# Kernel optimization log

Hardware: AMD Instinct MI355X
Metric: run time of the kernel (lower is better)

## Reference

```python
import jax, jax.numpy as jnp
import numpy as np

NUM_HEADS = 16
LN_EPS = 1e-5
ROPE_BASE = 10000.0


def setup_inputs() -> dict:
    key = jax.random.key(0)
    ks = jax.random.split(key, 4)
    B, T, D = 2, 2048, 1024
    return {
        "x": jax.random.normal(ks[0], (B, T, D), jnp.float32),
        "in_proj_weight": jax.random.normal(ks[1], (3 * D, D), jnp.float32) * 0.02,
        "in_proj_bias": jnp.zeros((3 * D,), jnp.float32),
        "out_proj_weight": jax.random.normal(ks[2], (D, D), jnp.float32) * 0.02,
        "out_proj_bias": jnp.zeros((D,), jnp.float32),
        "ln_gamma": jnp.ones((D,), jnp.float32),
        "ln_beta": jnp.zeros((D,), jnp.float32),
    }


def _rope_cos_sin(T, head_dim):
    # standard rotary tables; apply_rotary in the source truncates the
    # concatenated (T, head_dim) tables back to (T, head_dim//2), so we
    # build the half-width tables directly.
    inv_freq = 1.0 / (ROPE_BASE ** (jnp.arange(0, head_dim, 2, dtype=jnp.float32) / head_dim))
    t = jnp.arange(T, dtype=jnp.float32)
    freqs = jnp.outer(t, inv_freq)  # (T, head_dim//2)
    return jnp.cos(freqs), jnp.sin(freqs)


def _apply_rotary(x, cos, sin):
    # x: (B, H, T, hD), split-half rotary variant
    x1, x2 = jnp.split(x, 2, axis=-1)
    cos = cos[None, None]
    sin = sin[None, None]
    return jnp.concatenate([x1 * cos - x2 * sin, x2 * cos + x1 * sin], axis=-1).astype(x.dtype)


def reference(x, in_proj_weight, in_proj_bias, out_proj_weight, out_proj_bias, ln_gamma, ln_beta):
    B, T, D = x.shape
    H = NUM_HEADS
    hD = D // H
    residual = x

    # pre-LN
    mu = jnp.mean(x, axis=-1, keepdims=True)
    var = jnp.var(x, axis=-1, keepdims=True)
    xn = (x - mu) / jnp.sqrt(var + LN_EPS) * ln_gamma + ln_beta

    w_q, w_k, w_v = jnp.split(in_proj_weight, 3, axis=0)
    b_q, b_k, b_v = jnp.split(in_proj_bias, 3, axis=0)

    # first (manual) projection with bias
    q = xn @ w_q.T + b_q
    k = xn @ w_k.T + b_k
    v = xn @ w_v.T + b_v

    # RoPE per head
    q = q.reshape(B, T, H, hD).transpose(0, 2, 1, 3)
    k = k.reshape(B, T, H, hD).transpose(0, 2, 1, 3)
    cos, sin = _rope_cos_sin(T, hD)
    q = _apply_rotary(q, cos, sin)
    k = _apply_rotary(k, cos, sin)
    q = q.transpose(0, 2, 1, 3).reshape(B, T, D)
    k = k.transpose(0, 2, 1, 3).reshape(B, T, D)

    # second projection inside multi_head_attention_forward
    # (use_separate_proj_weight=True, in_proj_bias=None -> bias-free)
    q = q @ w_q.T
    k = k @ w_k.T
    v = v @ w_v.T

    q = q.reshape(B, T, H, hD).transpose(0, 2, 1, 3) * (hD ** -0.5)
    k = k.reshape(B, T, H, hD).transpose(0, 2, 1, 3)
    v = v.reshape(B, T, H, hD).transpose(0, 2, 1, 3)

    scores = jnp.einsum('bhtd,bhsd->bhts', q, k)
    causal = jnp.triu(jnp.full((T, T), -jnp.inf, dtype=scores.dtype), k=1)
    attn_weights = jax.nn.softmax(scores + causal, axis=-1)  # (B, H, T, T)

    out = jnp.einsum('bhts,bhsd->bhtd', attn_weights, v)
    out = out.transpose(0, 2, 1, 3).reshape(B, T, D)
    out = out @ out_proj_weight.T + out_proj_bias
    return out + residual, attn_weights
```

## Files before the change

### kernel.cpp

```cpp
#include <hip/hip_runtime.h>
#include <math.h>
#include <stdint.h>

typedef unsigned short u16;
typedef __bf16 bf16x8 __attribute__((ext_vector_type(8)));
typedef float f32x4 __attribute__((ext_vector_type(4)));

constexpr int Tq = 2048;
constexpr int D  = 1024;
constexpr int NHc = 16;
constexpr int Bc = 2;
constexpr int Mrows = Bc * Tq;

__device__ __forceinline__ float wsum(float v){
#pragma unroll
  for(int o=32;o;o>>=1) v += __shfl_xor(v,o);
  return v;
}
__device__ __forceinline__ u16 f2bf(float f){
  union{ float f; unsigned u; } v; v.f = f;
  unsigned r = v.u + 0x7fffu + ((v.u >> 16) & 1u);
  return (u16)(r >> 16);
}
__device__ __forceinline__ float bf2f(u16 b){
  union{ unsigned u; float f; } v; v.u = ((unsigned)b) << 16;
  return v.f;
}
__device__ __forceinline__ void gl2lds16(const void* g, void* l){
  __builtin_amdgcn_global_load_lds(
      (const __attribute__((address_space(1))) unsigned int*)g,
      (__attribute__((address_space(3))) unsigned int*)l, 16, 0, 0);
}

__global__ __launch_bounds__(256) void cvt_kernel(const float* __restrict__ s,
                                                  u16* __restrict__ d){
  const int i = blockIdx.x*256 + threadIdx.x;
  const float4 v = ((const float4*)s)[i];
  ushort4 o; o.x=f2bf(v.x); o.y=f2bf(v.y); o.z=f2bf(v.z); o.w=f2bf(v.w);
  ((ushort4*)d)[i] = o;
}

__global__ __launch_bounds__(256) void ln_kernel(const float* __restrict__ x,
    const float* __restrict__ g, const float* __restrict__ b,
    u16* __restrict__ xn){
  const int row = blockIdx.x;
  const int tid = threadIdx.x;
  const float4 v = ((const float4*)(x + (size_t)row*D))[tid];
  float s = v.x+v.y+v.z+v.w;
  float q = v.x*v.x+v.y*v.y+v.z*v.z+v.w*v.w;
  s = wsum(s); q = wsum(q);
  __shared__ float sb[4], qb[4];
  if((tid&63)==0){ sb[tid>>6]=s; qb[tid>>6]=q; }
  __syncthreads();
  const float ts = sb[0]+sb[1]+sb[2]+sb[3];
  const float tq = qb[0]+qb[1]+qb[2]+qb[3];
  const float mu   = ts*(1.0f/D);
  const float var  = tq*(1.0f/D) - mu*mu;
  const float rstd = rsqrtf(var + 1e-5f);
  const float4 gv = ((const float4*)g)[tid];
  const float4 bv = ((const float4*)b)[tid];
  ushort4 o;
  o.x = f2bf((v.x-mu)*rstd*gv.x + bv.x);
  o.y = f2bf((v.y-mu)*rstd*gv.y + bv.y);
  o.z = f2bf((v.z-mu)*rstd*gv.z + bv.z);
  o.w = f2bf((v.w-mu)*rstd*gv.w + bv.w);
  ((ushort4*)(xn + (size_t)row*D))[tid] = o;
}

template<int MODE>
__global__ __launch_bounds__(256) void gemm_bf16(
    const u16* __restrict__ A, const u16* __restrict__ B, void* __restrict__ Cv,
    const float* __restrict__ bias, const float* __restrict__ resid,
    int K, int lda, int ldb, int ldc){
  __shared__ __align__(16) u16 As[128*32];
  __shared__ __align__(16) u16 Bs[128*32];
  const int tid  = threadIdx.x;
  const int lane = tid & 63, wv = tid >> 6;
  const int wRow = (wv >> 1) * 64, wCol = (wv & 1) * 64;
  const int mBase = blockIdx.y*128, nBase = blockIdx.x*128;
  const int quad = lane >> 4, r16 = lane & 15;
  const int sRow = lane >> 2;
  const int sCol = (lane & 3) * 8;
  const char* smemA = (const char*)As;
  const char* smemB = (const char*)Bs;

  f32x4 acc[4][4];
#pragma unroll
  for(int i=0;i<4;i++)
#pragma unroll
    for(int j=0;j<4;j++) acc[i][j] = (f32x4)(0.f);

  for(int k0=0;k0<K;k0+=32){
#pragma unroll
    for(int rdn=0;rdn<2;rdn++){
      const int row = rdn*64 + wv*16 + sRow;
      gl2lds16(A + (size_t)(mBase + row)*lda + k0 + sCol,
               (void*)((char*)As + rdn*4096 + wv*1024));
      gl2lds16(B + (size_t)(nBase + row)*ldb + k0 + sCol,
               (void*)((char*)Bs + rdn*4096 + wv*1024));
    }
    __syncthreads();
    bf16x8 af[4], bfr[4];
#pragma unroll
    for(int i=0;i<4;i++)
      af[i]  = *(const bf16x8*)(smemA + (wRow + i*16 + r16)*64 + quad*16);
#pragma unroll
    for(int j=0;j<4;j++)
      bfr[j] = *(const bf16x8*)(smemB + (wCol + j*16 + r16)*64 + quad*16);
#pragma unroll
    for(int i=0;i<4;i++)
#pragma unroll
      for(int j=0;j<4;j++)
        acc[i][j] = __builtin_amdgcn_mfma_f32_16x16x32_bf16(af[i], bfr[j], acc[i][j], 0,0,0);
    __syncthreads();
  }

#pragma unroll
  for(int i=0;i<4;i++){
#pragma unroll
    for(int j=0;j<4;j++){
      const int n = nBase + wCol + j*16 + r16;
      if(MODE==0){
        u16* C = (u16*)Cv;
        const float bv = bias ? bias[n] : 0.f;
#pragma unroll
        for(int reg=0;reg<4;reg++){
          const int m = mBase + wRow + i*16 + quad*4 + reg;
          C[(size_t)m*ldc + n] = f2bf(acc[i][j][reg] + bv);
        }
      } else {
        float* C = (float*)Cv;
        const float bv = bias[n];
#pragma unroll
        for(int reg=0;reg<4;reg++){
          const int m = mBase + wRow + i*16 + quad*4 + reg;
          C[(size_t)m*ldc + n] = acc[i][j][reg] + bv + resid[(size_t)m*ldc + n];
        }
      }
    }
  }
}

__global__ __launch_bounds__(256) void rope_kernel(u16* __restrict__ q,
                                                   u16* __restrict__ k){
  const int idx = blockIdx.x*256 + threadIdx.x;
  const int m = idx >> 9;
  const int r = idx & 511;
  const int h = r >> 5, i = r & 31;
  const int t = m & (Tq-1);
  const float inv_freq = powf(10000.0f, -(float)i*(1.0f/32.0f));
  const float ang = (float)t * inv_freq;
  const float c = cosf(ang), s = sinf(ang);
  const size_t base = (size_t)m*D + h*64 + i;
  const float a0=bf2f(q[base]), a1=bf2f(q[base+32]);
  q[base]    = f2bf(a0*c - a1*s);
  q[base+32] = f2bf(a1*c + a0*s);
  const float b0=bf2f(k[base]), b1=bf2f(k[base+32]);
  k[base]    = f2bf(b0*c - b1*s);
  k[base+32] = f2bf(b1*c + b0*s);
}

__global__ __launch_bounds__(256) void transpose_v(const u16* __restrict__ v2,
                                                   u16* __restrict__ Vt){
  __shared__ u16 tile[64][65];
  const int bt = blockIdx.x;
  const int bh = blockIdx.y;
  const int b = bh >> 4, h = bh & 15;
  const int tid = threadIdx.x;
  const int t0 = bt*64;
#pragma unroll
  for(int rep=0;rep<4;rep++){
    const int tl = rep*16 + (tid>>4);
    const int dl = (tid&15)*4;
    const ushort4 val = *(const ushort4*)(v2 + (size_t)((size_t)b*Tq + t0 + tl)*D + h*64 + dl);
    tile[tl][dl+0]=val.x; tile[tl][dl+1]=val.y; tile[tl][dl+2]=val.z; tile[tl][dl+3]=val.w;
  }
  __syncthreads();
#pragma unroll
  for(int rep=0;rep<4;rep++){
    const int dl = rep*16 + (tid>>4);
    const int tl = (tid&15)*4;
    ushort4 o;
    o.x=tile[tl+0][dl]; o.y=tile[tl+1][dl]; o.z=tile[tl+2][dl]; o.w=tile[tl+3][dl];
    *(ushort4*)(Vt + ((size_t)bh*64 + dl)*Tq + t0 + tl) = o;
  }
}

__global__ __launch_bounds__(256, 2) void attn_fused(
    const u16* __restrict__ q2, const u16* __restrict__ k2,
    const u16* __restrict__ Vt, float* __restrict__ attnW,
    u16* __restrict__ O){
  constexpr int PSS = 40;
  __shared__ __align__(16) u16 Ks[2*128*32];
  __shared__ __align__(16) u16 Vs[4*64*32];
  __shared__ __align__(16) u16 QPs[2*128*32];

  const int n    = blockIdx.x + 16*blockIdx.y;
  const int tRow = (n >> 3) & 15;
  const int bh   = (n & 7) + 8*(n >> 7);
  const int b = bh >> 4, h = bh & 15;
  const int tid = threadIdx.x, lane = tid & 63, w = tid >> 6;
  const int quad = lane >> 4, r16 = lane & 15;
  const u16* Qg = q2 + ((size_t)b*Tq + (size_t)tRow*128)*D + h*64;
  const u16* Kg = k2 + ((size_t)b*Tq)*D + h*64;
  const u16* Vg = Vt + (size_t)bh*64*Tq;
  float* Wg = attnW + (size_t)bh*Tq*Tq + (size_t)tRow*128*Tq;

  for(int ct2 = tRow+1; ct2 < Tq/128; ++ct2){
#pragma unroll
    for(int it=0; it<16; ++it){
      const int r = it*8 + (tid>>5);
      ((f32x4*)(Wg + (size_t)r*Tq + ct2*128))[tid & 31] = (f32x4)(0.f);
    }
  }

#pragma unroll
  for(int rep=0; rep<4; ++rep){
    const int kb = rep*4 + w;
    const int kk = kb >> 3, row = (kb&7)*16 + (lane>>2);
    gl2lds16(Qg + (size_t)row*D + kk*32 + (lane&3)*8,
             (void*)((char*)QPs + kb*1024));
  }
  __syncthreads();
  bf16x8 af[2][2];
#pragma unroll
  for(int i=0;i<2;i++)
#pragma unroll
    for(int kk=0;kk<2;kk++)
      af[i][kk] = *(const bf16x8*)((const char*)QPs + kk*8192
                    + (w*32 + i*16 + r16)*64 + quad*16);

  float m[2][4], l[2][4];
#pragma unroll
  for(int i=0;i<2;i++)
#pragma unroll
    for(int rg=0;rg<4;rg++){ m[i][rg] = -1e30f; l[i][rg] = 0.f; }

  for(int ct=0; ct<=tRow; ++ct){
#pragma unroll
    for(int rep=0; rep<4; ++rep){
      const int kb = rep*4 + w;
      const int kk = kb >> 3, row = (kb&7)*16 + (lane>>2);
      gl2lds16(Kg + ((size_t)ct*128 + row)*D + kk*32 + (lane&3)*8,
               (void*)((char*)Ks + kb*1024));
    }
    __syncthreads();
    f32x4 acc[2][8];
#pragma unroll
    for(int i=0;i<2;i++)
#pragma unroll
      for(int j=0;j<8;j++) acc[i][j] = (f32x4)(0.f);
#pragma unroll
    for(int kk=0;kk<2;kk++){
#pragma unroll
      for(int j=0;j<8;j++){
        const bf16x8 bfj = *(const bf16x8*)((const char*)Ks + kk*8192
                             + (j*16 + r16)*64 + quad*16);
#pragma unroll
        for(int i=0;i<2;i++)
          acc[i][j] = __builtin_amdgcn_mfma_f32_16x16x32_bf16(af[i][kk], bfj, acc[i][j],0,0,0);
      }
    }
    const bool diag = (ct == tRow);
#pragma unroll
    for(int i=0;i<2;i++){
#pragma unroll
      for(int rg=0; rg<4; ++rg){
        const int rowg = w*32 + i*16 + quad*4 + rg;
        float sv[8]; float mx = -1e30f;
#pragma unroll
        for(int j=0;j<8;j++){
          float s = acc[i][j][rg]*0.125f;
          if(diag && (j*16 + r16) > rowg) s = -1e30f;
          sv[j]=s; mx = fmaxf(mx,s);
        }
#pragma unroll
        for(int o=8;o;o>>=1) mx = fmaxf(mx, __shfl_xor(mx,o));
        const float mn = fmaxf(m[i][rg], mx);
        float ls = 0.f;
#pragma unroll
        for(int j=0;j<8;j++) ls += __expf(sv[j]-mn);
#pragma unroll
        for(int o=8;o;o>>=1) ls += __shfl_xor(ls,o);
        l[i][rg] = l[i][rg]*__expf(m[i][rg]-mn) + ls;
        m[i][rg] = mn;
      }
    }
    __syncthreads();
  }

  float rinv[2][4];
#pragma unroll
  for(int i=0;i<2;i++)
#pragma unroll
    for(int rg=0;rg<4;rg++) rinv[i][rg] = 1.0f / l[i][rg];
  f32x4 oacc[2][4];
#pragma unroll
  for(int i=0;i<2;i++)
#pragma unroll
    for(int j=0;j<4;j++) oacc[i][j] = (f32x4)(0.f);

  char* psb = (char*)QPs + w*(32*PSS*2);

  for(int ct=0; ct<=tRow; ++ct){
#pragma unroll
    for(int rep=0; rep<4; ++rep){
      const int kb = rep*4 + w;
      const int kk = kb >> 3, row = (kb&7)*16 + (lane>>2);
      gl2lds16(Kg + ((size_t)ct*128 + row)*D + kk*32 + (lane&3)*8,
               (void*)((char*)Ks + kb*1024));
      const int vrow = w*16 + (lane>>2);
      gl2lds16(Vg + (size_t)vrow*Tq + ct*128 + rep*32 + (lane&3)*8,
               (void*)((char*)Vs + (rep*4 + w)*1024));
    }
    __syncthreads();
    f32x4 acc[2][8];
#pragma unroll
    for(int i=0;i<2;i++)
#pragma unroll
      for(int j=0;j<8;j++) acc[i][j] = (f32x4)(0.f);
#pragma unroll
    for(int kk=0;kk<2;kk++){
#pragma unroll
      for(int j=0;j<8;j++){
        const bf16x8 bfj = *(const bf16x8*)((const char*)Ks + kk*8192
                             + (j*16 + r16)*64 + quad*16);
#pragma unroll
        for(int i=0;i<2;i++)
          acc[i][j] = __builtin_amdgcn_mfma_f32_16x16x32_bf16(af[i][kk], bfj, acc[i][j],0,0,0);
      }
    }
    const bool diag = (ct == tRow);
#pragma unroll
    for(int c=0;c<4;c++){
#pragma unroll
      for(int i=0;i<2;i++){
#pragma unroll
        for(int jj=0;jj<2;jj++){
          const int j = c*2 + jj;
#pragma unroll
          for(int rg=0;rg<4;rg++){
            const int rowl = i*16 + quad*4 + rg;
            const int rowg = w*32 + rowl;
            float s = acc[i][j][rg]*0.125f;
            if(diag && (j*16 + r16) > rowg) s = -1e30f;
            const float p = __expf(s - m[i][rg]) * rinv[i][rg];
            Wg[(size_t)rowg*Tq + ct*128 + j*16 + r16] = p;
            *(u16*)(psb + rowl*(PSS*2) + (jj*16 + r16)*2) = f2bf(p);
          }
        }
      }
      asm volatile("s_waitcnt lgkmcnt(0)" ::: "memory");
      __builtin_amdgcn_sched_barrier(0);
      bf16x8 pa[2];
#pragma unroll
      for(int i=0;i<2;i++)
        pa[i] = *(const bf16x8*)(psb + (i*16 + r16)*(PSS*2) + quad*16);
#pragma unroll
      for(int j2=0;j2<4;j2++){
        const bf16x8 bv = *(const bf16x8*)((const char*)Vs + c*4096
                            + (j2*16 + r16)*64 + quad*16);
        oacc[0][j2] = __builtin_amdgcn_mfma_f32_16x16x32_bf16(pa[0], bv, oacc[0][j2],0,0,0);
        oacc[1][j2] = __builtin_amdgcn_mfma_f32_16x16x32_bf16(pa[1], bv, oacc[1][j2],0,0,0);
      }
      asm volatile("s_waitcnt lgkmcnt(0)" ::: "memory");
      __builtin_amdgcn_sched_barrier(0);
    }
    __syncthreads();
  }

#pragma unroll
  for(int i=0;i<2;i++)
#pragma unroll
    for(int j2=0;j2<4;j2++)
#pragma unroll
      for(int rg=0;rg<4;rg++){
        const int trow = tRow*128 + w*32 + i*16 + quad*4 + rg;
        O[((size_t)b*Tq + trow)*D + h*64 + j2*16 + r16] = f2bf(oacc[i][j2][rg]);
      }
}

extern "C" void kernel_launch(void* const* d_in, const int* in_sizes, int n_in,
                              void* d_out, int out_size, void* d_ws, size_t ws_size,
                              hipStream_t stream){
  const float* x    = (const float*)d_in[0];
  const float* Win  = (const float*)d_in[1];
  const float* bin  = (const float*)d_in[2];
  const float* Wout = (const float*)d_in[3];
  const float* bout = (const float*)d_in[4];
  const float* gam  = (const float*)d_in[5];
  const float* bet  = (const float*)d_in[6];

  float* out   = (float*)d_out;
  float* attnW = out + (size_t)Mrows*D;

  const size_t MB = 1u<<20;
  char* ws = (char*)d_ws;
  u16* Winb  = (u16*)(ws + 0);
  u16* Woutb = (u16*)(ws + 6*MB);
  u16* xn    = (u16*)(ws + 8*MB);
  u16* Vt    = xn;
  u16* q1    = (u16*)(ws + 16*MB);
  u16* Oat   = q1;
  u16* k1    = (u16*)(ws + 24*MB);
  u16* v1    = (u16*)(ws + 32*MB);
  u16* q2    = (u16*)(ws + 40*MB);
  u16* k2    = (u16*)(ws + 48*MB);
  u16* v2    = (u16*)(ws + 56*MB);

  const size_t DD = (size_t)D*D;

  cvt_kernel<<<(3*DD/4)/256, 256, 0, stream>>>(Win, Winb);
  cvt_kernel<<<(DD/4)/256, 256, 0, stream>>>(Wout, Woutb);

  ln_kernel<<<Mrows, 256, 0, stream>>>(x, gam, bet, xn);

  const dim3 gp(D/128, Mrows/128, 1);
  gemm_bf16<0><<<gp,256,0,stream>>>(xn, Winb,        q1, bin,      nullptr, D, D, D, D);
  gemm_bf16<0><<<gp,256,0,stream>>>(xn, Winb+DD,     k1, bin+D,    nullptr, D, D, D, D);
  gemm_bf16<0><<<gp,256,0,stream>>>(xn, Winb+2*DD,   v1, bin+2*D,  nullptr, D, D, D, D);

  rope_kernel<<<(Mrows*512)/256, 256, 0, stream>>>(q1, k1);

  gemm_bf16<0><<<gp,256,0,stream>>>(q1, Winb,        q2, nullptr, nullptr, D, D, D, D);
  gemm_bf16<0><<<gp,256,0,stream>>>(k1, Winb+DD,     k2, nullptr, nullptr, D, D, D, D);
  gemm_bf16<0><<<gp,256,0,stream>>>(v1, Winb+2*DD,   v2, nullptr, nullptr, D, D, D, D);

  transpose_v<<<dim3(Tq/64, Bc*NHc), 256, 0, stream>>>(v2, Vt);

  attn_fused<<<dim3(Tq/128, Bc*NHc), 256, 0, stream>>>(q2, k2, Vt, attnW, Oat);

  gemm_bf16<1><<<gp,256,0,stream>>>(Oat, Woutb, out, bout, x, D, D, D, D);
}
```

Before: 882.5 us.

## Batch QKV projections into single launches and fuse RoPE into GEMM epilogue

The three first-stage Q/K/V projections become one GEMM over the stacked 3D weight, with bias and rotary embedding applied in the epilogue from a precomputed cos/sin table. This removes the standalone RoPE pass over q and k. The three second-stage projections also run as one launch over stacked inputs and weights. This cuts launch count and gives each launch a larger grid for better CU fill, at the cost of extra table reads in the epilogue and more specialised kernels.

```diff
diff --git a/kernel.cpp b/kernel.cpp
--- a/kernel.cpp
+++ b/kernel.cpp
@@ -67,11 +67,18 @@
   ((ushort4*)(xn + (size_t)row*D))[tid] = o;
 }
 
-template<int MODE>
-__global__ __launch_bounds__(256) void gemm_bf16(
-    const u16* __restrict__ A, const u16* __restrict__ B, void* __restrict__ Cv,
-    const float* __restrict__ bias, const float* __restrict__ resid,
-    int K, int lda, int ldb, int ldc){
+__global__ __launch_bounds__(256) void rope_tab_kernel(float2* __restrict__ tab){
+  const int idx = blockIdx.x*256 + threadIdx.x;
+  const int t = idx >> 5, fi = idx & 31;
+  const float inv = powf(10000.0f, -(float)fi*(1.0f/32.0f));
+  const float ang = (float)t * inv;
+  tab[idx] = make_float2(cosf(ang), sinf(ang));
+}
+
+__global__ __launch_bounds__(256) void gemm_qkv1(
+    const u16* __restrict__ A, const u16* __restrict__ B,
+    const float* __restrict__ bias, const float2* __restrict__ tab,
+    u16* __restrict__ out){
   __shared__ __align__(16) u16 As[128*32];
   __shared__ __align__(16) u16 Bs[128*32];
   const int tid  = threadIdx.x;
@@ -90,13 +97,13 @@
 #pragma unroll
     for(int j=0;j<4;j++) acc[i][j] = (f32x4)(0.f);
 
-  for(int k0=0;k0<K;k0+=32){
+  for(int k0=0;k0<D;k0+=32){
 #pragma unroll
     for(int rdn=0;rdn<2;rdn++){
       const int row = rdn*64 + wv*16 + sRow;
-      gl2lds16(A + (size_t)(mBase + row)*lda + k0 + sCol,
+      gl2lds16(A + (size_t)(mBase + row)*D + k0 + sCol,
                (void*)((char*)As + rdn*4096 + wv*1024));
-      gl2lds16(B + (size_t)(nBase + row)*ldb + k0 + sCol,
+      gl2lds16(B + (size_t)(nBase + row)*D + k0 + sCol,
                (void*)((char*)Bs + rdn*4096 + wv*1024));
     }
     __syncthreads();
@@ -115,49 +122,168 @@
     __syncthreads();
   }
 
+  const int sel  = nBase >> 10;
+  const int nLoc = nBase & 1023;
+  u16* C = out + (size_t)sel*Mrows*D;
+  if(sel < 2){
+#pragma unroll
+    for(int i=0;i<4;i++){
+#pragma unroll
+      for(int jp=0;jp<2;jp++){
+        const int hp  = jp*16 + r16;
+        const int col = nLoc + wCol + hp;
+        const float bv0 = bias[nBase + wCol + hp];
+        const float bv1 = bias[nBase + wCol + hp + 32];
+#pragma unroll
+        for(int reg=0;reg<4;reg++){
+          const int mm = mBase + wRow + i*16 + quad*4 + reg;
+          const float2 cs = tab[((mm & (Tq-1))<<5) + hp];
+          const float a0 = acc[i][jp][reg]   + bv0;
+          const float a1 = acc[i][jp+2][reg] + bv1;
+          C[(size_t)mm*D + col]      = f2bf(a0*cs.x - a1*cs.y);
+          C[(size_t)mm*D + col + 32] = f2bf(a1*cs.x + a0*cs.y);
+        }
+      }
+    }
+  } else {
+#pragma unroll
+    for(int i=0;i<4;i++){
+#pragma unroll
+      for(int j=0;j<4;j++){
+        const int n = nBase + wCol + j*16 + r16;
+        const float bv = bias[n];
+        const int col = nLoc + wCol + j*16 + r16;
+#pragma unroll
+        for(int reg=0;reg<4;reg++){
+          const int mm = mBase + wRow + i*16 + quad*4 + reg;
+          C[(size_t)mm*D + col] = f2bf(acc[i][j][reg] + bv);
+        }
+      }
+    }
+  }
+}
+
+__global__ __launch_bounds__(256) void gemm_stack3(
+    const u16* __restrict__ A, const u16* __restrict__ Bw,
+    u16* __restrict__ C){
+  __shared__ __align__(16) u16 As[128*32];
+  __shared__ __align__(16) u16 Bs[128*32];
+  const int wsel = blockIdx.y >> 5;
+  const u16* B = Bw + (size_t)wsel*D*D;
+  const int tid  = threadIdx.x;
+  const int lane = tid & 63, wv = tid >> 6;
+  const int wRow = (wv >> 1) * 64, wCol = (wv & 1) * 64;
+  const int mBase = blockIdx.y*128, nBase = blockIdx.x*128;
+  const int quad = lane >> 4, r16 = lane & 15;
+  const int sRow = lane >> 2;
+  const int sCol = (lane & 3) * 8;
+  const char* smemA = (const char*)As;
+  const char* smemB = (const char*)Bs;
+
+  f32x4 acc[4][4];
+#pragma unroll
+  for(int i=0;i<4;i++)
+#pragma unroll
+    for(int j=0;j<4;j++) acc[i][j] = (f32x4)(0.f);
+
+  for(int k0=0;k0<D;k0+=32){
+#pragma unroll
+    for(int rdn=0;rdn<2;rdn++){
+      const int row = rdn*64 + wv*16 + sRow;
+      gl2lds16(A + (size_t)(mBase + row)*D + k0 + sCol,
+               (void*)((char*)As + rdn*4096 + wv*1024));
+      gl2lds16(B + (size_t)(nBase + row)*D + k0 + sCol,
+               (void*)((char*)Bs + rdn*4096 + wv*1024));
+    }
+    __syncthreads();
+    bf16x8 af[4], bfr[4];
+#pragma unroll
+    for(int i=0;i<4;i++)
+      af[i]  = *(const bf16x8*)(smemA + (wRow + i*16 + r16)*64 + quad*16);
+#pragma unroll
+    for(int j=0;j<4;j++)
+      bfr[j] = *(const bf16x8*)(smemB + (wCol + j*16 + r16)*64 + quad*16);
+#pragma unroll
+    for(int i=0;i<4;i++)
+#pragma unroll
+      for(int j=0;j<4;j++)
+        acc[i][j] = __builtin_amdgcn_mfma_f32_16x16x32_bf16(af[i], bfr[j], acc[i][j], 0,0,0);
+    __syncthreads();
+  }
+
 #pragma unroll
   for(int i=0;i<4;i++){
 #pragma unroll
     for(int j=0;j<4;j++){
       const int n = nBase + wCol + j*16 + r16;
-      if(MODE==0){
-        u16* C = (u16*)Cv;
-        const float bv = bias ? bias[n] : 0.f;
-#pragma unroll
-        for(int reg=0;reg<4;reg++){
-          const int m = mBase + wRow + i*16 + quad*4 + reg;
-          C[(size_t)m*ldc + n] = f2bf(acc[i][j][reg] + bv);
-        }
-      } else {
-        float* C = (float*)Cv;
-        const float bv = bias[n];
-#pragma unroll
-        for(int reg=0;reg<4;reg++){
-          const int m = mBase + wRow + i*16 + quad*4 + reg;
-          C[(size_t)m*ldc + n] = acc[i][j][reg] + bv + resid[(size_t)m*ldc + n];
-        }
-      }
-    }
-  }
-}
-
-__global__ __launch_bounds__(256) void rope_kernel(u16* __restrict__ q,
-                                                   u16* __restrict__ k){
-  const int idx = blockIdx.x*256 + threadIdx.x;
-  const int m = idx >> 9;
-  const int r = idx & 511;
-  const int h = r >> 5, i = r & 31;
-  const int t = m & (Tq-1);
-  const float inv_freq = powf(10000.0f, -(float)i*(1.0f/32.0f));
-  const float ang = (float)t * inv_freq;
-  const float c = cosf(ang), s = sinf(ang);
-  const size_t base = (size_t)m*D + h*64 + i;
-  const float a0=bf2f(q[base]), a1=bf2f(q[base+32]);
-  q[base]    = f2bf(a0*c - a1*s);
-  q[base+32] = f2bf(a1*c + a0*s);
-  const float b0=bf2f(k[base]), b1=bf2f(k[base+32]);
-  k[base]    = f2bf(b0*c - b1*s);
-  k[base+32] = f2bf(b1*c + b0*s);
+#pragma unroll
+      for(int reg=0;reg<4;reg++){
+        const int mm = mBase + wRow + i*16 + quad*4 + reg;
+        C[(size_t)mm*D + n] = f2bf(acc[i][j][reg]);
+      }
+    }
+  }
+}
+
+__global__ __launch_bounds__(256) void gemm_out(
+    const u16* __restrict__ A, const u16* __restrict__ B, float* __restrict__ C,
+    const float* __restrict__ bias, const float* __restrict__ resid){
+  __shared__ __align__(16) u16 As[128*32];
+  __shared__ __align__(16) u16 Bs[128*32];
+  const int tid  = threadIdx.x;
+  const int lane = tid & 63, wv = tid >> 6;
+  const int wRow = (wv >> 1) * 64, wCol = (wv & 1) * 64;
+  const int mBase = blockIdx.y*128, nBase = blockIdx.x*128;
+  const int quad = lane >> 4, r16 = lane & 15;
+  const int sRow = lane >> 2;
+  const int sCol = (lane & 3) * 8;
+  const char* smemA = (const char*)As;
+  const char* smemB = (const char*)Bs;
+
+  f32x4 acc[4][4];
+#pragma unroll
+  for(int i=0;i<4;i++)
+#pragma unroll
+    for(int j=0;j<4;j++) acc[i][j] = (f32x4)(0.f);
+
+  for(int k0=0;k0<D;k0+=32){
+#pragma unroll
+    for(int rdn=0;rdn<2;rdn++){
+      const int row = rdn*64 + wv*16 + sRow;
+      gl2lds16(A + (size_t)(mBase + row)*D + k0 + sCol,
+               (void*)((char*)As + rdn*4096 + wv*1024));
+      gl2lds16(B + (size_t)(nBase + row)*D + k0 + sCol,
+               (void*)((char*)Bs + rdn*4096 + wv*1024));
+    }
+    __syncthreads();
+    bf16x8 af[4], bfr[4];
+#pragma unroll
+    for(int i=0;i<4;i++)
+      af[i]  = *(const bf16x8*)(smemA + (wRow + i*16 + r16)*64 + quad*16);
+#pragma unroll
+    for(int j=0;j<4;j++)
+      bfr[j] = *(const bf16x8*)(smemB + (wCol + j*16 + r16)*64 + quad*16);
+#pragma unroll
+    for(int i=0;i<4;i++)
+#pragma unroll
+      for(int j=0;j<4;j++)
+        acc[i][j] = __builtin_amdgcn_mfma_f32_16x16x32_bf16(af[i], bfr[j], acc[i][j], 0,0,0);
+    __syncthreads();
+  }
+
+#pragma unroll
+  for(int i=0;i<4;i++){
+#pragma unroll
+    for(int j=0;j<4;j++){
+      const int n = nBase + wCol + j*16 + r16;
+      const float bv = bias[n];
+#pragma unroll
+      for(int reg=0;reg<4;reg++){
+        const int mm = mBase + wRow + i*16 + quad*4 + reg;
+        C[(size_t)mm*D + n] = acc[i][j][reg] + bv + resid[(size_t)mm*D + n];
+      }
+    }
+  }
 }
 
 __global__ __launch_bounds__(256) void transpose_v(const u16* __restrict__ v2,
@@ -400,35 +526,29 @@
   u16* Woutb = (u16*)(ws + 6*MB);
   u16* xn    = (u16*)(ws + 8*MB);
   u16* Vt    = xn;
-  u16* q1    = (u16*)(ws + 16*MB);
-  u16* Oat   = q1;
-  u16* k1    = (u16*)(ws + 24*MB);
-  u16* v1    = (u16*)(ws + 32*MB);
-  u16* q2    = (u16*)(ws + 40*MB);
-  u16* k2    = (u16*)(ws + 48*MB);
-  u16* v2    = (u16*)(ws + 56*MB);
+  u16* qkv1  = (u16*)(ws + 16*MB);
+  u16* Oat   = qkv1;
+  u16* qkv2  = (u16*)(ws + 40*MB);
+  float2* tab = (float2*)(ws + 40*MB);
 
   const size_t DD = (size_t)D*D;
+  const u16* q2 = qkv2;
+  const u16* k2 = qkv2 + (size_t)Mrows*D;
+  const u16* v2 = qkv2 + 2*(size_t)Mrows*D;
 
   cvt_kernel<<<(3*DD/4)/256, 256, 0, stream>>>(Win, Winb);
   cvt_kernel<<<(DD/4)/256, 256, 0, stream>>>(Wout, Woutb);
+  rope_tab_kernel<<<(Tq*32)/256, 256, 0, stream>>>(tab);
 
   ln_kernel<<<Mrows, 256, 0, stream>>>(x, gam, bet, xn);
 
-  const dim3 gp(D/128, Mrows/128, 1);
-  gemm_bf16<0><<<gp,256,0,stream>>>(xn, Winb,        q1, bin,      nullptr, D, D, D, D);
-  gemm_bf16<0><<<gp,256,0,stream>>>(xn, Winb+DD,     k1, bin+D,    nullptr, D, D, D, D);
-  gemm_bf16<0><<<gp,256,0,stream>>>(xn, Winb+2*DD,   v1, bin+2*D,  nullptr, D, D, D, D);
-
-  rope_kernel<<<(Mrows*512)/256, 256, 0, stream>>>(q1, k1);
-
-  gemm_bf16<0><<<gp,256,0,stream>>>(q1, Winb,        q2, nullptr, nullptr, D, D, D, D);
-  gemm_bf16<0><<<gp,256,0,stream>>>(k1, Winb+DD,     k2, nullptr, nullptr, D, D, D, D);
-  gemm_bf16<0><<<gp,256,0,stream>>>(v1, Winb+2*DD,   v2, nullptr, nullptr, D, D, D, D);
+  gemm_qkv1<<<dim3(3*D/128, Mrows/128), 256, 0, stream>>>(xn, Winb, bin, tab, qkv1);
+
+  gemm_stack3<<<dim3(D/128, 3*Mrows/128), 256, 0, stream>>>(qkv1, Winb, qkv2);
 
   transpose_v<<<dim3(Tq/64, Bc*NHc), 256, 0, stream>>>(v2, Vt);
 
   attn_fused<<<dim3(Tq/128, Bc*NHc), 256, 0, stream>>>(q2, k2, Vt, attnW, Oat);
 
-  gemm_bf16<1><<<gp,256,0,stream>>>(Oat, Woutb, out, bout, x, D, D, D, D);
-}
+  gemm_out<<<dim3(D/128, Mrows/128), 256, 0, stream>>>(Oat, Woutb, out, bout, x);
+}
```

Result: faster. 796.2 us (-9.8%).
